# Kernel optimization log

Measured on AMD Instinct MI355X. Metric: run time of the kernel, lower is better.

The kernel has to match this reference:

```python
import jax, jax.numpy as jnp
import numpy as np
from jax import lax

B, N, C_IN = 16, 4096, 128
C_HID, N_CLS = 128, 10
DS = 32          # sparse_map_downsample
G = 4096 // DS   # quantized grid extent = 128


def setup_inputs() -> dict:
    key = jax.random.key(0)
    k = jax.random.split(key, 6)
    x = jax.random.normal(k[0], (B, N, C_IN), dtype=jnp.float32)
    coords = jax.random.randint(k[1], (B, N, 2), 0, 4096, dtype=jnp.int32)
    W1 = jax.random.normal(k[2], (3, 3, C_IN, C_HID), dtype=jnp.float32) * (1.0 / np.sqrt(9 * C_IN))
    W2 = jax.random.normal(k[3], (3, 3, C_HID, C_HID), dtype=jnp.float32) * (1.0 / np.sqrt(9 * C_HID))
    Wc = jax.random.normal(k[4], (C_HID, N_CLS), dtype=jnp.float32) * (1.0 / np.sqrt(C_HID))
    bc = jnp.zeros((N_CLS,), dtype=jnp.float32)
    return {"x": x, "coords": coords, "W1": W1, "W2": W2, "Wc": Wc, "bc": bc}


def reference(x, coords, W1, W2, Wc, bc):
    # --- coordinate quantization (tl / downsample, floored to int) ---
    q = jnp.floor(coords.astype(jnp.float32) / DS).astype(jnp.int32)  # [B,N,2] in [0,G)
    lin = q[..., 0] * G + q[..., 1]                                   # [B,N]
    seg = (jnp.arange(B, dtype=jnp.int32)[:, None] * (G * G) + lin).reshape(-1)  # [B*N]

    # --- UNWEIGHTED_AVERAGE quantization: average features colliding in a cell ---
    feats = x.reshape(-1, C_IN)
    sums = jax.ops.segment_sum(feats, seg, num_segments=B * G * G)            # [B*G*G, C]
    counts = jax.ops.segment_sum(jnp.ones((B * N,), x.dtype), seg, num_segments=B * G * G)
    grid = (sums / jnp.maximum(counts, 1.0)[:, None]).reshape(B, G, G, C_IN)  # dense sparse-map
    mask = (counts > 0).astype(x.dtype).reshape(B, G, G, 1)                   # occupancy

    # --- two sparse 3x3 convs (stride 1, no bias) + ReLU; outputs live only at
    #     occupied coordinates, so mask after each conv ---
    def sconv(g, W):
        y = lax.conv_general_dilated(g, W, window_strides=(1, 1), padding='SAME',
                                     dimension_numbers=('NHWC', 'HWIO', 'NHWC'))
        return jax.nn.relu(y) * mask

    h = sconv(grid, W1)
    h = sconv(h, W2)

    # --- MinkowskiGlobalAvgPooling: mean over occupied coordinates per bag ---
    npts = jnp.sum(mask, axis=(1, 2))            # [B,1]
    pooled = jnp.sum(h, axis=(1, 2)) / npts      # [B,C_HID]

    # --- MinkowskiLinear classifier ---
    logits = pooled @ Wc + bc                    # [B,N_CLS]
    return logits
```

## Files before the change

### kernel.cpp

```cpp
#include <hip/hip_runtime.h>
#include <hip/hip_bf16.h>

#define GG 16384
#define NBAG 16
#define NPT 65536
#define NCELL (NBAG * GG)
#define MAXM NPT
#define ZROW MAXM

typedef __bf16 bf16x8 __attribute__((ext_vector_type(8)));
typedef float f32x4 __attribute__((ext_vector_type(4)));

__global__ __launch_bounds__(256) void k_zero(int* __restrict__ counts,
                                              float* __restrict__ pooled,
                                              int* __restrict__ dcnt,
                                              __hip_bfloat16* __restrict__ feat0,
                                              __hip_bfloat16* __restrict__ feat1) {
  int tid = blockIdx.x * 256 + threadIdx.x;
  int4 z = make_int4(0, 0, 0, 0);
  ((int4*)counts)[tid] = z;
  if (tid < 512) ((int4*)pooled)[tid] = z;
  if (tid == 513) { dcnt[0] = 0; dcnt[1] = 0; dcnt[2] = 0; dcnt[3] = 0; }
  if (tid >= 1024 && tid < 1040)
    ((int4*)(feat0 + (size_t)ZROW * 128))[tid - 1024] = z;
  if (tid >= 1056 && tid < 1072)
    ((int4*)(feat1 + (size_t)ZROW * 128))[tid - 1056] = z;
}

__global__ __launch_bounds__(256) void k_setup(const float* __restrict__ W1,
                                               const float* __restrict__ W2,
                                               __hip_bfloat16* __restrict__ Wt1,
                                               __hip_bfloat16* __restrict__ Wt2,
                                               const int* __restrict__ coords,
                                               int* __restrict__ counts) {
  int b = blockIdx.x, t = threadIdx.x;
  if (b < 1152) {
    int id = b * 256 + t;
    const float* W = (id < 147456) ? W1 : W2;
    __hip_bfloat16* Wt = (id < 147456) ? Wt1 : Wt2;
    int r = (id < 147456) ? id : id - 147456;
    int k = r >> 14, rem = r & 16383, co = rem >> 7, ci = rem & 127;
    int dst = k * 16384 + co * 128 + (((ci >> 3) ^ (co & 7)) << 3) + (ci & 7);
    Wt[dst] = __float2bfloat16(W[k * 16384 + ci * 128 + co]);
  } else {
    int p = (b - 1152) * 256 + t;
    int bg = p >> 12;
    int q0 = coords[p * 2 + 0] >> 5;
    int q1 = coords[p * 2 + 1] >> 5;
    atomicAdd(&counts[bg * GG + q0 * 128 + q1], 1);
  }
}

__global__ __launch_bounds__(256) void k_scan(const int* __restrict__ counts,
                                              int* __restrict__ blockcnt,
                                              int* __restrict__ blockoff,
                                              int* __restrict__ dM,
                                              int* __restrict__ npts,
                                              int* __restrict__ dcnt) {
  __shared__ int red[256];
  __shared__ int isLast;
  int t = threadIdx.x;
  int base = blockIdx.x * 1024 + t * 4;
  int c = 0;
#pragma unroll
  for (int i = 0; i < 4; ++i) c += (counts[base + i] > 0) ? 1 : 0;
  red[t] = c;
  __syncthreads();
  for (int d = 128; d > 0; d >>= 1) {
    if (t < d) red[t] += red[t + d];
    __syncthreads();
  }
  if (t == 0) {
    blockcnt[blockIdx.x] = red[0];
    __threadfence();
    isLast = (atomicAdd(&dcnt[0], 1) == 255);
  }
  __syncthreads();
  if (!isLast) return;
  __threadfence();
  int v = blockcnt[t];
  red[t] = v;
  __syncthreads();
  for (int d = 1; d < 256; d <<= 1) {
    int x = (t >= d) ? red[t - d] : 0;
    __syncthreads();
    red[t] += x;
    __syncthreads();
  }
  blockoff[t] = red[t] - v;
  if (t == 255) *dM = red[255];
  if (t < NBAG) {
    int sum = 0;
    for (int i = 0; i < 16; ++i) sum += blockcnt[t * 16 + i];
    npts[t] = sum;
  }
}

__global__ __launch_bounds__(256) void k_s3(const int* __restrict__ counts,
                                            const int* __restrict__ blockoff,
                                            int* __restrict__ cellidx,
                                            int* __restrict__ cell_of_idx,
                                            float* __restrict__ fsum) {
  __shared__ int s[256];
  int t = threadIdx.x;
  int base = blockIdx.x * 1024 + t * 4;
  int occ[4];
  int c = 0;
#pragma unroll
  for (int i = 0; i < 4; ++i) {
    occ[i] = counts[base + i] > 0;
    c += occ[i];
  }
  s[t] = c;
  __syncthreads();
  for (int d = 1; d < 256; d <<= 1) {
    int x = (t >= d) ? s[t - d] : 0;
    __syncthreads();
    s[t] += x;
    __syncthreads();
  }
  int pos = blockoff[blockIdx.x] + s[t] - c;
  int4 z = make_int4(0, 0, 0, 0);
#pragma unroll
  for (int i = 0; i < 4; ++i) {
    if (occ[i]) {
      cellidx[base + i] = pos;
      cell_of_idx[pos] = base + i;
      if (counts[base + i] > 1) {
        int4* fz = (int4*)(fsum + (size_t)pos * 128);
#pragma unroll
        for (int j = 0; j < 32; ++j) fz[j] = z;
      }
      pos++;
    } else {
      cellidx[base + i] = -1;
    }
  }
}

__global__ __launch_bounds__(256) void k_gather(const float* __restrict__ x,
                                                const int* __restrict__ coords,
                                                const int* __restrict__ cellidx,
                                                const int* __restrict__ counts,
                                                const int* __restrict__ cell_of_idx,
                                                const int* __restrict__ dM,
                                                float* __restrict__ fsum,
                                                __hip_bfloat16* __restrict__ feat0,
                                                int* __restrict__ nbrt) {
  int b = blockIdx.x, t = threadIdx.x;
  if (b < 8192) {
    int gid = b * 256 + t;
    int p = gid >> 5, c4 = gid & 31;
    int bg = p >> 12;
    int q0 = coords[p * 2 + 0] >> 5;
    int q1 = coords[p * 2 + 1] >> 5;
    int cell = bg * GG + q0 * 128 + q1;
    int idx = cellidx[cell];
    float4 v = ((const float4*)x)[(size_t)p * 32 + c4];
    if (counts[cell] == 1) {
      __align__(8) __hip_bfloat16 h[4];
      h[0] = __float2bfloat16(v.x);
      h[1] = __float2bfloat16(v.y);
      h[2] = __float2bfloat16(v.z);
      h[3] = __float2bfloat16(v.w);
      *(int2*)(feat0 + (size_t)idx * 128 + c4 * 4) = *(const int2*)h;
    } else {
      float* dst = fsum + (size_t)idx * 128 + c4 * 4;
      atomicAdd(dst + 0, v.x);
      atomicAdd(dst + 1, v.y);
      atomicAdd(dst + 2, v.z);
      atomicAdd(dst + 3, v.w);
    }
  } else {
    int idx = (b - 8192) * 256 + t;
    if (idx >= *dM) {
#pragma unroll
      for (int j = 0; j < 9; ++j) nbrt[j * MAXM + idx] = ZROW;
      return;
    }
    int cell = cell_of_idx[idx];
    int bb = cell >> 14, ij = cell & 16383;
    int i = ij >> 7, j = ij & 127;
#pragma unroll
    for (int dh = 0; dh < 3; ++dh)
#pragma unroll
      for (int dw = 0; dw < 3; ++dw) {
        int ni = i + dh - 1, nj = j + dw - 1;
        int v = -1;
        if (ni >= 0 && ni < 128 && nj >= 0 && nj < 128)
          v = cellidx[bb * GG + ni * 128 + nj];
        nbrt[(dh * 3 + dw) * MAXM + idx] = (v < 0) ? ZROW : v;
      }
  }
}

__global__ __launch_bounds__(256) void k_avg(const float* __restrict__ fsum,
                                             const int* __restrict__ counts,
                                             const int* __restrict__ cell_of_idx,
                                             const int* __restrict__ dM,
                                             __hip_bfloat16* __restrict__ feat0) {
  int gid = blockIdx.x * 256 + threadIdx.x;
  int cell = gid >> 4, i = gid & 15;
  if (cell >= *dM) return;
  int cnt = counts[cell_of_idx[cell]];
  if (cnt == 1) return;
  float inv = 1.0f / (float)cnt;
  const float4* src = (const float4*)fsum + (size_t)cell * 32 + i * 2;
  float4 v0 = src[0], v1 = src[1];
  __align__(16) __hip_bfloat16 h[8];
  h[0] = __float2bfloat16(v0.x * inv);
  h[1] = __float2bfloat16(v0.y * inv);
  h[2] = __float2bfloat16(v0.z * inv);
  h[3] = __float2bfloat16(v0.w * inv);
  h[4] = __float2bfloat16(v1.x * inv);
  h[5] = __float2bfloat16(v1.y * inv);
  h[6] = __float2bfloat16(v1.z * inv);
  h[7] = __float2bfloat16(v1.w * inv);
  *(int4*)(feat0 + (size_t)cell * 128 + i * 8) = *(const int4*)h;
}

template <bool POOL>
__global__ __launch_bounds__(256, 2) void k_conv(
    const __hip_bfloat16* __restrict__ fin,
    const __hip_bfloat16* __restrict__ Wt,
    __hip_bfloat16* __restrict__ fout,
    float* __restrict__ pooled,
    const int* __restrict__ nbrt,
    const int* __restrict__ cell_of_idx,
    const int* __restrict__ dM) {
  __shared__ __align__(16) char smem[65536];
  const int M = *dM;
  const int lb = (blockIdx.x & 7) * (gridDim.x >> 3) + (blockIdx.x >> 3);
  const int base = lb * 128;
  if (base >= M) return;
  const int t = threadIdx.x;
  const int w = t >> 6;
  const int l = t & 63;
  const int u = l >> 4;
  const int c = l & 15;
  const int wrow = base + w * 32;

  auto stageW = [&](int k, int b) {
    const __hip_bfloat16* gw = Wt + (size_t)k * 16384 + w * 4096;
    char* lbuf = smem + b * 32768 + w * 8192;
#pragma unroll
    for (int j = 0; j < 8; ++j) {
      __builtin_amdgcn_global_load_lds(
          (const __attribute__((address_space(1))) void*)(gw + j * 512 + l * 8),
          (__attribute__((address_space(3))) void*)(lbuf + j * 1024), 16, 0, 0);
    }
  };
  auto loadA = [&](int nb, int kb) {
    return *(const bf16x8*)((const char*)fin + (size_t)nb * 256 + kb * 64 + u * 16);
  };

  f32x4 acc[2][8];
#pragma unroll
  for (int mf = 0; mf < 2; ++mf)
#pragma unroll
    for (int nf = 0; nf < 8; ++nf) acc[mf][nf] = f32x4{0.f, 0.f, 0.f, 0.f};

  bf16x8 aP[2][2][4];
  int nb_c[2], nb_n[2];
  nb_c[0] = nbrt[0 * MAXM + wrow + c];
  nb_c[1] = nbrt[0 * MAXM + wrow + 16 + c];
  nb_n[0] = nbrt[1 * MAXM + wrow + c];
  nb_n[1] = nbrt[1 * MAXM + wrow + 16 + c];
  stageW(0, 0);
  __builtin_amdgcn_sched_barrier(0);
#pragma unroll
  for (int mf = 0; mf < 2; ++mf)
#pragma unroll
    for (int kb = 0; kb < 4; ++kb) aP[0][mf][kb] = loadA(nb_c[mf], kb);

#pragma unroll
  for (int k = 0; k < 9; ++k) {
    const int cp = k & 1, np = cp ^ 1;
    if (k == 0) {
      asm volatile("s_waitcnt vmcnt(8)" ::: "memory");
    } else {
      asm volatile("s_waitcnt vmcnt(10)" ::: "memory");
    }
    __builtin_amdgcn_s_barrier();
    if (k < 8) {
      stageW(k + 1, (k + 1) & 1);
      __builtin_amdgcn_sched_barrier(0);
#pragma unroll
      for (int mf = 0; mf < 2; ++mf)
#pragma unroll
        for (int kb = 0; kb < 4; ++kb) aP[np][mf][kb] = loadA(nb_n[mf], kb);
      const int kk = (k + 2 > 8) ? 0 : (k + 2);
      nb_n[0] = nbrt[kk * MAXM + wrow + c];
      nb_n[1] = nbrt[kk * MAXM + wrow + 16 + c];
    }
    const char* wb = smem + (k & 1) * 32768;
    __builtin_amdgcn_s_setprio(1);
#pragma unroll
    for (int kb = 0; kb < 4; ++kb) {
      bf16x8 wf[8];
#pragma unroll
      for (int nf = 0; nf < 8; ++nf) {
        int co = nf * 16 + c;
        int ch = (kb * 4 + u) ^ (c & 7);
        wf[nf] = *(const bf16x8*)(wb + co * 256 + ch * 16);
      }
#pragma unroll
      for (int mf = 0; mf < 2; ++mf)
#pragma unroll
        for (int nf = 0; nf < 8; ++nf)
          acc[mf][nf] = __builtin_amdgcn_mfma_f32_16x16x32_bf16(
              aP[cp][mf][kb], wf[nf], acc[mf][nf], 0, 0, 0);
    }
    __builtin_amdgcn_s_setprio(0);
  }
  __syncthreads();

  if (!POOL) {
    char* ep = smem + w * 8704;
#pragma unroll
    for (int mf = 0; mf < 2; ++mf)
#pragma unroll
      for (int nf = 0; nf < 8; ++nf)
#pragma unroll
        for (int i = 0; i < 4; ++i) {
          int rl = mf * 16 + u * 4 + i;
          int col = nf * 16 + c;
          *(__hip_bfloat16*)(ep + rl * 272 + col * 2) =
              __float2bfloat16(fmaxf(acc[mf][nf][i], 0.f));
        }
    __syncthreads();
#pragma unroll
    for (int j = 0; j < 8; ++j) {
      int rl = j * 4 + u;
      int grow = wrow + rl;
      int4 v = *(const int4*)(ep + rl * 272 + c * 16);
      if (grow < M)
        *(int4*)((char*)fout + (size_t)grow * 256 + c * 16) = v;
    }
  } else {
    if (wrow < M) {
      int b0 = cell_of_idx[wrow] >> 14;
      int lastr = min(wrow + 31, M - 1);
      int b1 = cell_of_idx[lastr] >> 14;
      float p0[8] = {0.f, 0.f, 0.f, 0.f, 0.f, 0.f, 0.f, 0.f};
      float p1[8] = {0.f, 0.f, 0.f, 0.f, 0.f, 0.f, 0.f, 0.f};
#pragma unroll
      for (int mf = 0; mf < 2; ++mf)
#pragma unroll
        for (int i = 0; i < 4; ++i) {
          int r = wrow + mf * 16 + u * 4 + i;
          int bg = (r < M) ? (cell_of_idx[r] >> 14) : -1;
#pragma unroll
          for (int nf = 0; nf < 8; ++nf) {
            float v = fmaxf(acc[mf][nf][i], 0.f);
            if (bg == b0) p0[nf] += v;
            else if (bg == b1) p1[nf] += v;
          }
        }
      bool two = (b1 != b0);
#pragma unroll
      for (int nf = 0; nf < 8; ++nf) {
        p0[nf] += __shfl_xor(p0[nf], 16);
        p0[nf] += __shfl_xor(p0[nf], 32);
        p1[nf] += __shfl_xor(p1[nf], 16);
        p1[nf] += __shfl_xor(p1[nf], 32);
      }
      if (u == 0) {
#pragma unroll
        for (int nf = 0; nf < 8; ++nf) {
          atomicAdd(&pooled[b0 * 128 + nf * 16 + c], p0[nf]);
          if (two) atomicAdd(&pooled[b1 * 128 + nf * 16 + c], p1[nf]);
        }
      }
    }
  }
}

__global__ __launch_bounds__(256) void k_logits(const float* __restrict__ pooled,
                                                const int* __restrict__ npts,
                                                const float* __restrict__ Wc,
                                                const float* __restrict__ bc,
                                                float* __restrict__ out) {
  int t = threadIdx.x;
  if (t >= 160) return;
  int b = t / 10, n = t % 10;
  float inv = 1.0f / (float)npts[b];
  float s = 0.f;
  for (int c = 0; c < 128; ++c) s += pooled[b * 128 + c] * Wc[c * 10 + n];
  out[t] = s * inv + bc[n];
}

extern "C" void kernel_launch(void* const* d_in, const int* in_sizes, int n_in,
                              void* d_out, int out_size, void* d_ws, size_t ws_size,
                              hipStream_t stream) {
  const float* x = (const float*)d_in[0];
  const int* coords = (const int*)d_in[1];
  const float* W1 = (const float*)d_in[2];
  const float* W2 = (const float*)d_in[3];
  const float* Wc = (const float*)d_in[4];
  const float* bc = (const float*)d_in[5];
  float* out = (float*)d_out;

  char* ws = (char*)d_ws;
  size_t off = 0;
  auto take = [&](size_t bytes) {
    void* p = ws + off;
    off += (bytes + 255) & ~(size_t)255;
    return p;
  };
  int* counts      = (int*)take((size_t)NCELL * 4);
  int* cellidx     = (int*)take((size_t)NCELL * 4);
  int* cell_of_idx = (int*)take((size_t)MAXM * 4);
  int* blockcnt    = (int*)take(256 * 4);
  int* blockoff    = (int*)take(256 * 4);
  int* dM          = (int*)take(4);
  int* npts        = (int*)take(64);
  int* dcnt        = (int*)take(64);
  int* nbrt        = (int*)take((size_t)9 * MAXM * 4);
  float* fsum      = (float*)take((size_t)MAXM * 128 * 4);
  __hip_bfloat16* feat0 = (__hip_bfloat16*)take((size_t)(MAXM + 1) * 128 * 2);
  __hip_bfloat16* feat1 = (__hip_bfloat16*)take((size_t)(MAXM + 1) * 128 * 2);
  __hip_bfloat16* Wt1   = (__hip_bfloat16*)take((size_t)9 * 128 * 128 * 2);
  __hip_bfloat16* Wt2   = (__hip_bfloat16*)take((size_t)9 * 128 * 128 * 2);
  float* pooled    = (float*)take(16 * 128 * 4);

  k_zero<<<256, 256, 0, stream>>>(counts, pooled, dcnt, feat0, feat1);
  k_setup<<<1408, 256, 0, stream>>>(W1, W2, Wt1, Wt2, coords, counts);
  k_scan<<<256, 256, 0, stream>>>(counts, blockcnt, blockoff, dM, npts, dcnt);
  k_s3<<<256, 256, 0, stream>>>(counts, blockoff, cellidx, cell_of_idx, fsum);
  k_gather<<<8448, 256, 0, stream>>>(x, coords, cellidx, counts, cell_of_idx, dM,
                                     fsum, feat0, nbrt);
  k_avg<<<4096, 256, 0, stream>>>(fsum, counts, cell_of_idx, dM, feat0);
  k_conv<false><<<MAXM / 128, 256, 0, stream>>>(feat0, Wt1, feat1, nullptr, nbrt,
                                                cell_of_idx, dM);
  k_conv<true><<<MAXM / 128, 256, 0, stream>>>(feat1, Wt2, nullptr, pooled, nbrt,
                                               cell_of_idx, dM);
  k_logits<<<1, 256, 0, stream>>>(pooled, npts, Wc, bc, out);
}
```

Measured before the change: 123.7 us.

## Fuse setup, scan and compaction kernels into one grid-barrier kernel

Merges the weight transpose/count histogram, block-count reduction and exclusive-scan compaction into a single persistent kernel of 256 blocks. The phases are separated by software grid barriers built on atomic counters. This removes two kernel launches and the 'last block' scan pattern. It relies on all 256 blocks being co-resident, otherwise the barriers deadlock. The conv loop also stops prefetching the neighbor index on the last iterations and uses a uniform vmcnt wait.

```diff
diff --git a/kernel.cpp b/kernel.cpp
--- a/kernel.cpp
+++ b/kernel.cpp
@@ -20,113 +20,114 @@
   int4 z = make_int4(0, 0, 0, 0);
   ((int4*)counts)[tid] = z;
   if (tid < 512) ((int4*)pooled)[tid] = z;
-  if (tid == 513) { dcnt[0] = 0; dcnt[1] = 0; dcnt[2] = 0; dcnt[3] = 0; }
+  if (tid < 4) ((int4*)dcnt)[tid] = z;
   if (tid >= 1024 && tid < 1040)
     ((int4*)(feat0 + (size_t)ZROW * 128))[tid - 1024] = z;
   if (tid >= 1056 && tid < 1072)
     ((int4*)(feat1 + (size_t)ZROW * 128))[tid - 1056] = z;
 }
 
-__global__ __launch_bounds__(256) void k_setup(const float* __restrict__ W1,
-                                               const float* __restrict__ W2,
-                                               __hip_bfloat16* __restrict__ Wt1,
-                                               __hip_bfloat16* __restrict__ Wt2,
-                                               const int* __restrict__ coords,
-                                               int* __restrict__ counts) {
-  int b = blockIdx.x, t = threadIdx.x;
-  if (b < 1152) {
-    int id = b * 256 + t;
-    const float* W = (id < 147456) ? W1 : W2;
-    __hip_bfloat16* Wt = (id < 147456) ? Wt1 : Wt2;
-    int r = (id < 147456) ? id : id - 147456;
-    int k = r >> 14, rem = r & 16383, co = rem >> 7, ci = rem & 127;
-    int dst = k * 16384 + co * 128 + (((ci >> 3) ^ (co & 7)) << 3) + (ci & 7);
-    Wt[dst] = __float2bfloat16(W[k * 16384 + ci * 128 + co]);
-  } else {
-    int p = (b - 1152) * 256 + t;
+__device__ __forceinline__ void gridbar(int* bar) {
+  __syncthreads();
+  if (threadIdx.x == 0) {
+    __threadfence();
+    atomicAdd(bar, 1);
+    while (atomicAdd(bar, 0) < 256) {}
+    __threadfence();
+  }
+  __syncthreads();
+}
+
+__global__ __launch_bounds__(256) void k_prep(const float* __restrict__ W1,
+                                              const float* __restrict__ W2,
+                                              __hip_bfloat16* __restrict__ Wt1,
+                                              __hip_bfloat16* __restrict__ Wt2,
+                                              const int* __restrict__ coords,
+                                              int* __restrict__ counts,
+                                              int* __restrict__ blockcnt,
+                                              int* __restrict__ dM,
+                                              int* __restrict__ npts,
+                                              int* __restrict__ dcnt,
+                                              int* __restrict__ cellidx,
+                                              int* __restrict__ cell_of_idx,
+                                              float* __restrict__ fsum) {
+  __shared__ int sh[256];
+  __shared__ int shoff;
+  const int b = blockIdx.x, t = threadIdx.x;
+  const int gid = b * 256 + t;
+
+  {
+    int p = gid;
     int bg = p >> 12;
     int q0 = coords[p * 2 + 0] >> 5;
     int q1 = coords[p * 2 + 1] >> 5;
     atomicAdd(&counts[bg * GG + q0 * 128 + q1], 1);
-  }
-}
-
-__global__ __launch_bounds__(256) void k_scan(const int* __restrict__ counts,
-                                              int* __restrict__ blockcnt,
-                                              int* __restrict__ blockoff,
-                                              int* __restrict__ dM,
-                                              int* __restrict__ npts,
-                                              int* __restrict__ dcnt) {
-  __shared__ int red[256];
-  __shared__ int isLast;
-  int t = threadIdx.x;
-  int base = blockIdx.x * 1024 + t * 4;
+    for (int id = gid; id < 2 * 147456; id += 65536) {
+      const float* W = (id < 147456) ? W1 : W2;
+      __hip_bfloat16* Wt = (id < 147456) ? Wt1 : Wt2;
+      int r = (id < 147456) ? id : id - 147456;
+      int k = r >> 14, rem = r & 16383, co = rem >> 7, ci = rem & 127;
+      int dst = k * 16384 + co * 128 + (((ci >> 3) ^ (co & 7)) << 3) + (ci & 7);
+      Wt[dst] = __float2bfloat16(W[k * 16384 + ci * 128 + co]);
+    }
+  }
+  gridbar(&dcnt[4]);
+
+  const int base = b * 1024 + t * 4;
+  int cnt4[4], occ[4];
   int c = 0;
 #pragma unroll
-  for (int i = 0; i < 4; ++i) c += (counts[base + i] > 0) ? 1 : 0;
-  red[t] = c;
+  for (int i = 0; i < 4; ++i) {
+    cnt4[i] = counts[base + i];
+    occ[i] = cnt4[i] > 0;
+    c += occ[i];
+  }
+  sh[t] = c;
   __syncthreads();
   for (int d = 128; d > 0; d >>= 1) {
-    if (t < d) red[t] += red[t + d];
-    __syncthreads();
-  }
-  if (t == 0) {
-    blockcnt[blockIdx.x] = red[0];
-    __threadfence();
-    isLast = (atomicAdd(&dcnt[0], 1) == 255);
-  }
-  __syncthreads();
-  if (!isLast) return;
-  __threadfence();
+    if (t < d) sh[t] += sh[t + d];
+    __syncthreads();
+  }
+  if (t == 0) blockcnt[b] = sh[0];
+  gridbar(&dcnt[5]);
+
   int v = blockcnt[t];
-  red[t] = v;
+  __syncthreads();
+  sh[t] = v;
   __syncthreads();
   for (int d = 1; d < 256; d <<= 1) {
-    int x = (t >= d) ? red[t - d] : 0;
-    __syncthreads();
-    red[t] += x;
-    __syncthreads();
-  }
-  blockoff[t] = red[t] - v;
-  if (t == 255) *dM = red[255];
-  if (t < NBAG) {
-    int sum = 0;
-    for (int i = 0; i < 16; ++i) sum += blockcnt[t * 16 + i];
-    npts[t] = sum;
-  }
-}
-
-__global__ __launch_bounds__(256) void k_s3(const int* __restrict__ counts,
-                                            const int* __restrict__ blockoff,
-                                            int* __restrict__ cellidx,
-                                            int* __restrict__ cell_of_idx,
-                                            float* __restrict__ fsum) {
-  __shared__ int s[256];
-  int t = threadIdx.x;
-  int base = blockIdx.x * 1024 + t * 4;
-  int occ[4];
-  int c = 0;
-#pragma unroll
-  for (int i = 0; i < 4; ++i) {
-    occ[i] = counts[base + i] > 0;
-    c += occ[i];
-  }
-  s[t] = c;
+    int x = (t >= d) ? sh[t - d] : 0;
+    __syncthreads();
+    sh[t] += x;
+    __syncthreads();
+  }
+  if (t == b) shoff = sh[t] - v;
+  if (b == 0) {
+    if (t == 255) *dM = sh[255];
+    if (t < NBAG) {
+      int sum = 0;
+      for (int i = 0; i < 16; ++i) sum += blockcnt[t * 16 + i];
+      npts[t] = sum;
+    }
+  }
+  __syncthreads();
+
+  sh[t] = c;
   __syncthreads();
   for (int d = 1; d < 256; d <<= 1) {
-    int x = (t >= d) ? s[t - d] : 0;
-    __syncthreads();
-    s[t] += x;
-    __syncthreads();
-  }
-  int pos = blockoff[blockIdx.x] + s[t] - c;
+    int x = (t >= d) ? sh[t - d] : 0;
+    __syncthreads();
+    sh[t] += x;
+    __syncthreads();
+  }
+  int pos = shoff + sh[t] - c;
   int4 z = make_int4(0, 0, 0, 0);
 #pragma unroll
   for (int i = 0; i < 4; ++i) {
     if (occ[i]) {
       cellidx[base + i] = pos;
       cell_of_idx[pos] = base + i;
-      if (counts[base + i] > 1) {
+      if (cnt4[i] > 1) {
         int4* fz = (int4*)(fsum + (size_t)pos * 128);
 #pragma unroll
         for (int j = 0; j < 32; ++j) fz[j] = z;
@@ -276,11 +277,7 @@
 #pragma unroll
   for (int k = 0; k < 9; ++k) {
     const int cp = k & 1, np = cp ^ 1;
-    if (k == 0) {
-      asm volatile("s_waitcnt vmcnt(8)" ::: "memory");
-    } else {
-      asm volatile("s_waitcnt vmcnt(10)" ::: "memory");
-    }
+    asm volatile("s_waitcnt vmcnt(8)" ::: "memory");
     __builtin_amdgcn_s_barrier();
     if (k < 8) {
       stageW(k + 1, (k + 1) & 1);
@@ -289,9 +286,10 @@
       for (int mf = 0; mf < 2; ++mf)
 #pragma unroll
         for (int kb = 0; kb < 4; ++kb) aP[np][mf][kb] = loadA(nb_n[mf], kb);
-      const int kk = (k + 2 > 8) ? 0 : (k + 2);
-      nb_n[0] = nbrt[kk * MAXM + wrow + c];
-      nb_n[1] = nbrt[kk * MAXM + wrow + 16 + c];
+    }
+    if (k < 7) {
+      nb_n[0] = nbrt[(k + 2) * MAXM + wrow + c];
+      nb_n[1] = nbrt[(k + 2) * MAXM + wrow + 16 + c];
     }
     const char* wb = smem + (k & 1) * 32768;
     __builtin_amdgcn_s_setprio(1);
@@ -412,7 +410,6 @@
   int* cellidx     = (int*)take((size_t)NCELL * 4);
   int* cell_of_idx = (int*)take((size_t)MAXM * 4);
   int* blockcnt    = (int*)take(256 * 4);
-  int* blockoff    = (int*)take(256 * 4);
   int* dM          = (int*)take(4);
   int* npts        = (int*)take(64);
   int* dcnt        = (int*)take(64);
@@ -425,9 +422,8 @@
   float* pooled    = (float*)take(16 * 128 * 4);
 
   k_zero<<<256, 256, 0, stream>>>(counts, pooled, dcnt, feat0, feat1);
-  k_setup<<<1408, 256, 0, stream>>>(W1, W2, Wt1, Wt2, coords, counts);
-  k_scan<<<256, 256, 0, stream>>>(counts, blockcnt, blockoff, dM, npts, dcnt);
-  k_s3<<<256, 256, 0, stream>>>(counts, blockoff, cellidx, cell_of_idx, fsum);
+  k_prep<<<256, 256, 0, stream>>>(W1, W2, Wt1, Wt2, coords, counts, blockcnt,
+                                  dM, npts, dcnt, cellidx, cell_of_idx, fsum);
   k_gather<<<8448, 256, 0, stream>>>(x, coords, cellidx, counts, cell_of_idx, dM,
                                      fsum, feat0, nbrt);
   k_avg<<<4096, 256, 0, stream>>>(fsum, counts, cell_of_idx, dM, feat0);
```

After: 155.3 us. 1.26x slower.
